# Kernel optimization log

Hardware: AMD Instinct MI355X
Metric: run time of the kernel (lower is better)

Reference implementation:

```python
import jax, jax.numpy as jnp
import numpy as np

B, T = 16384, 128
PI = np.pi
MAX_ITERS = 1000


def _quat_to_mat(q):
    # pytorch3d quaternion_to_matrix, q is (..., 4) wxyz
    w, x, y, z = q[..., 0], q[..., 1], q[..., 2], q[..., 3]
    two = 2.0 / jnp.sum(q * q, axis=-1)
    r00 = 1.0 - two * (y * y + z * z)
    r01 = two * (x * y - z * w)
    r02 = two * (x * z + y * w)
    r10 = two * (x * y + z * w)
    r11 = 1.0 - two * (x * x + z * z)
    r12 = two * (y * z - x * w)
    r20 = two * (x * z - y * w)
    r21 = two * (y * z + x * w)
    r22 = 1.0 - two * (x * x + y * y)
    return jnp.stack([
        jnp.stack([r00, r01, r02], -1),
        jnp.stack([r10, r11, r12], -1),
        jnp.stack([r20, r21, r22], -1)], -2)


def _mat_to_quat(m):
    # pytorch3d matrix_to_quaternion, m is (..., 3, 3) -> (..., 4) wxyz
    m00, m01, m02 = m[..., 0, 0], m[..., 0, 1], m[..., 0, 2]
    m10, m11, m12 = m[..., 1, 0], m[..., 1, 1], m[..., 1, 2]
    m20, m21, m22 = m[..., 2, 0], m[..., 2, 1], m[..., 2, 2]
    q_abs = jnp.sqrt(jnp.clip(jnp.stack([
        1.0 + m00 + m11 + m22,
        1.0 + m00 - m11 - m22,
        1.0 - m00 + m11 - m22,
        1.0 - m00 - m11 + m22], -1), 1e-8))
    cand = jnp.stack([
        jnp.stack([q_abs[..., 0] ** 2, m21 - m12, m02 - m20, m10 - m01], -1),
        jnp.stack([m21 - m12, q_abs[..., 1] ** 2, m01 + m10, m02 + m20], -1),
        jnp.stack([m02 - m20, m10 + m01, q_abs[..., 2] ** 2, m12 + m21], -1),
        jnp.stack([m10 - m01, m20 + m02, m21 + m12, q_abs[..., 3] ** 2], -1)], -2)
    cand = cand / (2.0 * jnp.maximum(q_abs[..., None], 0.1))
    best = jnp.argmax(q_abs, axis=-1)
    return jnp.take_along_axis(cand, best[..., None, None], axis=-2)[..., 0, :]


def _build_R(key, batch, dtype):
    k = jax.random.split(key, 4)
    ax = jax.random.uniform(k[0], (batch,), dtype) * 2 * PI - PI
    ay = jax.random.uniform(k[1], (batch,), dtype) * 2 * PI - PI
    az = jax.random.uniform(k[2], (batch,), dtype) * 2 * PI - PI
    mask = jax.random.uniform(k[3], (batch,), dtype) < (1.0 / 64.0)
    ax = jnp.where(mask, 0.0, ax)
    ay = jnp.where(mask, 0.0, ay)
    az = jnp.where(mask, 0.0, az)
    cx, sx = jnp.cos(ax), jnp.sin(ax)
    cy, sy = jnp.cos(ay), jnp.sin(ay)
    cz, sz = jnp.cos(az), jnp.sin(az)
    o, z0 = jnp.ones_like(ax), jnp.zeros_like(ax)
    Rx = jnp.stack([jnp.stack([o, z0, z0], -1), jnp.stack([z0, cx, -sx], -1), jnp.stack([z0, sx, cx], -1)], -2)
    Ry = jnp.stack([jnp.stack([cy, z0, sy], -1), jnp.stack([z0, o, z0], -1), jnp.stack([-sy, z0, cy], -1)], -2)
    Rz = jnp.stack([jnp.stack([cz, -sz, z0], -1), jnp.stack([sz, cz, z0], -1), jnp.stack([z0, z0, o], -1)], -2)
    return Rz @ Ry @ Rx  # [B, 3, 3]


def setup_inputs() -> dict:
    key = jax.random.key(0)
    kp, kq = jax.random.split(key)
    # positions scaled to (-0.5, 0.5): every point has norm < 1 so rotated
    # components stay in [-1, 1] and the acceptance test passes
    pos = (jax.random.uniform(kp, (B, T, 3), jnp.float32) * 2.0 - 1.0) * 0.5
    quat = jax.random.normal(kq, (B, T, 4), jnp.float32)
    quat = quat / jnp.linalg.norm(quat, axis=-1, keepdims=True)
    return {"pos": pos, "quat": quat}


def reference(pos, quat):
    batch = pos.shape[0]
    quat_wxyz = quat[..., jnp.array([3, 0, 1, 2])]
    eye = jnp.broadcast_to(jnp.eye(3, dtype=pos.dtype), (batch, 3, 3))

    def cond(s):
        i, key, acc, R = s
        return jnp.logical_and(~acc, i < MAX_ITERS)

    def body(s):
        i, key, acc, R = s
        key, sub = jax.random.split(key)
        Rn = _build_R(sub, batch, pos.dtype)
        rp = jnp.einsum('bij,btj->bti', Rn, pos)
        ok = jnp.logical_and(rp.min() >= -1.0, rp.max() <= 1.0)
        return (i + 1, key, ok, Rn)

    i, _, acc, R = jax.lax.while_loop(
        cond, body, (jnp.int32(0), jax.random.key(42), jnp.bool_(False), eye))
    # torch code falls back to identity if it exhausted all 1000 tries
    # (including acceptance on the very last iteration, matching `if i == 999`)
    use_id = i >= MAX_ITERS
    Rf = jnp.where(use_id, eye, R)
    rotated_pos = jnp.einsum('bij,btj->bti', Rf, pos)
    rot = _quat_to_mat(quat_wxyz)                       # [B,T,3,3]
    rotated_rot = jnp.einsum('bij,btjk->btik', Rf, rot)
    rotated_quat = _mat_to_quat(rotated_rot)[..., jnp.array([1, 2, 3, 0])]  # back to xyzw
    pos_out = jnp.where(use_id, pos, rotated_pos)
    quat_out = jnp.where(use_id, quat, rotated_quat)
    return pos_out, quat_out, Rf
```

## Files before the change

### kernel.cpp

```cpp
#include <hip/hip_runtime.h>
#include <stdint.h>

#define B_DIM 16384
#define T_DIM 128

struct U2 { uint32_t a, b; };

__host__ __device__ constexpr uint32_t rotl32c(uint32_t x, uint32_t n) {
    return (x << n) | (x >> (32u - n));
}

__host__ __device__ constexpr U2 tf(uint32_t k0, uint32_t k1,
                                    uint32_t x0, uint32_t x1) {
    uint32_t ks2 = k0 ^ k1 ^ 0x1BD11BDAu;
    x0 += k0; x1 += k1;
#define RND(r) { x0 += x1; x1 = rotl32c(x1, r); x1 ^= x0; }
    RND(13) RND(15) RND(26) RND(6)
    x0 += k1; x1 += ks2 + 1u;
    RND(17) RND(29) RND(16) RND(24)
    x0 += ks2; x1 += k0 + 2u;
    RND(13) RND(15) RND(26) RND(6)
    x0 += k0; x1 += k1 + 3u;
    RND(17) RND(29) RND(16) RND(24)
    x0 += k1; x1 += ks2 + 4u;
    RND(13) RND(15) RND(26) RND(6)
    x0 += ks2; x1 += k0 + 5u;
#undef RND
    return U2{x0, x1};
}

constexpr U2 SUB = tf(0u, 42u, 0u, 1u);
constexpr U2 K0 = tf(SUB.a, SUB.b, 0u, 0u);
constexpr U2 K1 = tf(SUB.a, SUB.b, 0u, 1u);
constexpr U2 K2 = tf(SUB.a, SUB.b, 0u, 2u);
constexpr U2 K3 = tf(SUB.a, SUB.b, 0u, 3u);

__device__ __forceinline__ float bits_to_uniform(uint32_t bits) {
    uint32_t u = (bits >> 9) | 0x3F800000u;
    return __uint_as_float(u) - 1.0f;
}

__device__ __forceinline__ uint32_t rbits(U2 k, uint32_t i) {
    U2 o = tf(k.a, k.b, 0u, i);
    return o.a ^ o.b;
}

__global__ void build_R_kernel(float* __restrict__ Rf) {
    int b = blockIdx.x * blockDim.x + threadIdx.x;
    if (b >= B_DIM) return;

    uint32_t bx = rbits(K0, (uint32_t)b);
    uint32_t by = rbits(K1, (uint32_t)b);
    uint32_t bz = rbits(K2, (uint32_t)b);
    uint32_t bm = rbits(K3, (uint32_t)b);

    const float PI_F = 3.14159265358979323846f;
    float ax = bits_to_uniform(bx) * 2.0f * PI_F - PI_F;
    float ay = bits_to_uniform(by) * 2.0f * PI_F - PI_F;
    float az = bits_to_uniform(bz) * 2.0f * PI_F - PI_F;
    bool mask = bits_to_uniform(bm) < 0.015625f;
    if (mask) { ax = 0.0f; ay = 0.0f; az = 0.0f; }

    float sx, cx, sy, cy, sz, cz;
    sincosf(ax, &sx, &cx);
    sincosf(ay, &sy, &cy);
    sincosf(az, &sz, &cz);

    float r00 = cz * cy;
    float r01 = cz * sy * sx - sz * cx;
    float r02 = cz * sy * cx + sz * sx;
    float r10 = sz * cy;
    float r11 = sz * sy * sx + cz * cx;
    float r12 = sz * sy * cx - cz * sx;
    float r20 = -sy;
    float r21 = cy * sx;
    float r22 = cy * cx;

    float* o = Rf + (size_t)b * 9;
    o[0] = r00; o[1] = r01; o[2] = r02;
    o[3] = r10; o[4] = r11; o[5] = r12;
    o[6] = r20; o[7] = r21; o[8] = r22;
}

__global__ __launch_bounds__(T_DIM) void rot_apply_kernel(
    const float* __restrict__ pos, const float* __restrict__ quat,
    const float* __restrict__ Rf, float* __restrict__ pos_out,
    float* __restrict__ quat_out) {
    __shared__ float Rs[9];
    int b = blockIdx.x;
    int t = threadIdx.x;
    if (t < 9) Rs[t] = Rf[(size_t)b * 9 + t];
    __syncthreads();
    float R00 = Rs[0], R01 = Rs[1], R02 = Rs[2];
    float R10 = Rs[3], R11 = Rs[4], R12 = Rs[5];
    float R20 = Rs[6], R21 = Rs[7], R22 = Rs[8];

    size_t idx = (size_t)b * T_DIM + t;

    const float* p = pos + idx * 3;
    float px = p[0], py = p[1], pz = p[2];
    float ox = R00 * px + R01 * py + R02 * pz;
    float oy = R10 * px + R11 * py + R12 * pz;
    float oz = R20 * px + R21 * py + R22 * pz;
    float* po = pos_out + idx * 3;
    po[0] = ox; po[1] = oy; po[2] = oz;

    float4 q = ((const float4*)quat)[idx];
    float qx = q.x, qy = q.y, qz = q.z, qw = q.w;
    float ss = qw * qw + qx * qx + qy * qy + qz * qz;
    float two = 2.0f / ss;
    float m00 = 1.0f - two * (qy * qy + qz * qz);
    float m01 = two * (qx * qy - qz * qw);
    float m02 = two * (qx * qz + qy * qw);
    float m10 = two * (qx * qy + qz * qw);
    float m11 = 1.0f - two * (qx * qx + qz * qz);
    float m12 = two * (qy * qz - qx * qw);
    float m20 = two * (qx * qz - qy * qw);
    float m21 = two * (qy * qz + qx * qw);
    float m22 = 1.0f - two * (qx * qx + qy * qy);

    float n00 = R00 * m00 + R01 * m10 + R02 * m20;
    float n01 = R00 * m01 + R01 * m11 + R02 * m21;
    float n02 = R00 * m02 + R01 * m12 + R02 * m22;
    float n10 = R10 * m00 + R11 * m10 + R12 * m20;
    float n11 = R10 * m01 + R11 * m11 + R12 * m21;
    float n12 = R10 * m02 + R11 * m12 + R12 * m22;
    float n20 = R20 * m00 + R21 * m10 + R22 * m20;
    float n21 = R20 * m01 + R21 * m11 + R22 * m21;
    float n22 = R20 * m02 + R21 * m12 + R22 * m22;

    float t0 = 1.0f + n00 + n11 + n22;
    float t1 = 1.0f + n00 - n11 - n22;
    float t2 = 1.0f - n00 + n11 - n22;
    float t3 = 1.0f - n00 - n11 + n22;
    float q0 = sqrtf(fmaxf(t0, 1e-8f));
    float q1 = sqrtf(fmaxf(t1, 1e-8f));
    float q2 = sqrtf(fmaxf(t2, 1e-8f));
    float q3 = sqrtf(fmaxf(t3, 1e-8f));

    int best = 0; float bv = q0;
    if (q1 > bv) { best = 1; bv = q1; }
    if (q2 > bv) { best = 2; bv = q2; }
    if (q3 > bv) { best = 3; bv = q3; }
    float denom = 2.0f * fmaxf(bv, 0.1f);

    float w, x, y, z;
    if (best == 0)      { w = q0 * q0;  x = n21 - n12; y = n02 - n20; z = n10 - n01; }
    else if (best == 1) { w = n21 - n12; x = q1 * q1;  y = n01 + n10; z = n02 + n20; }
    else if (best == 2) { w = n02 - n20; x = n10 + n01; y = q2 * q2;  z = n12 + n21; }
    else                { w = n10 - n01; x = n20 + n02; y = n21 + n12; z = q3 * q3;  }

    float4 qo;
    qo.x = x / denom; qo.y = y / denom; qo.z = z / denom; qo.w = w / denom;
    ((float4*)quat_out)[idx] = qo;
}

extern "C" void kernel_launch(void* const* d_in, const int* in_sizes, int n_in,
                              void* d_out, int out_size, void* d_ws, size_t ws_size,
                              hipStream_t stream) {
    const float* pos  = (const float*)d_in[0];
    const float* quat = (const float*)d_in[1];
    float* out = (float*)d_out;
    float* pos_out  = out;
    float* quat_out = out + (size_t)B_DIM * T_DIM * 3;
    float* Rf       = out + (size_t)B_DIM * T_DIM * 7;

    build_R_kernel<<<(B_DIM + 255) / 256, 256, 0, stream>>>(Rf);
    rot_apply_kernel<<<B_DIM, T_DIM, 0, stream>>>(pos, quat, Rf, pos_out, quat_out);
}
```

Measured before the change: 110.5 us.

## Stage pos through LDS for coalesced float4 I/O and process two batches per block

The apply kernel now loads each batch's position data into shared memory with float4 reads and writes the rotated positions back through shared memory as float4 stores. This replaces strided 3-float accesses per thread. Each block handles two batch rows with 256 threads. The build kernel uses 64-thread blocks to spread work over more CUs, and the four quaternion divides become one reciprocal plus multiplies. The cost is a second barrier and extra LDS traffic.

```diff
diff --git a/kernel.cpp b/kernel.cpp
--- a/kernel.cpp
+++ b/kernel.cpp
@@ -3,6 +3,8 @@
 
 #define B_DIM 16384
 #define T_DIM 128
+#define NB 2
+#define BLK (NB * T_DIM)
 
 struct U2 { uint32_t a, b; };
 
@@ -45,7 +47,7 @@
     return o.a ^ o.b;
 }
 
-__global__ void build_R_kernel(float* __restrict__ Rf) {
+__global__ __launch_bounds__(64) void build_R_kernel(float* __restrict__ Rf) {
     int b = blockIdx.x * blockDim.x + threadIdx.x;
     if (b >= B_DIM) return;
 
@@ -82,28 +84,36 @@
     o[6] = r20; o[7] = r21; o[8] = r22;
 }
 
-__global__ __launch_bounds__(T_DIM) void rot_apply_kernel(
+__global__ __launch_bounds__(BLK) void rot_apply_kernel(
     const float* __restrict__ pos, const float* __restrict__ quat,
     const float* __restrict__ Rf, float* __restrict__ pos_out,
     float* __restrict__ quat_out) {
-    __shared__ float Rs[9];
-    int b = blockIdx.x;
-    int t = threadIdx.x;
-    if (t < 9) Rs[t] = Rf[(size_t)b * 9 + t];
+    __shared__ float Ps[NB * T_DIM * 3];
+    __shared__ float Rs[NB * 9];
+
+    const int t  = threadIdx.x;
+    const int b0 = blockIdx.x * NB;
+
+    if (t < NB * 9) Rs[t] = Rf[(size_t)b0 * 9 + t];
+
+    const float4* pin = (const float4*)(pos + (size_t)b0 * T_DIM * 3);
+    if (t < NB * T_DIM * 3 / 4) ((float4*)Ps)[t] = pin[t];
     __syncthreads();
-    float R00 = Rs[0], R01 = Rs[1], R02 = Rs[2];
-    float R10 = Rs[3], R11 = Rs[4], R12 = Rs[5];
-    float R20 = Rs[6], R21 = Rs[7], R22 = Rs[8];
 
-    size_t idx = (size_t)b * T_DIM + t;
+    const int lb = t >> 7;
+    const int e  = t & (T_DIM - 1);
+    const size_t idx = (size_t)(b0 + lb) * T_DIM + e;
+    const int pofs = lb * (T_DIM * 3) + e * 3;
 
-    const float* p = pos + idx * 3;
-    float px = p[0], py = p[1], pz = p[2];
-    float ox = R00 * px + R01 * py + R02 * pz;
-    float oy = R10 * px + R11 * py + R12 * pz;
-    float oz = R20 * px + R21 * py + R22 * pz;
-    float* po = pos_out + idx * 3;
-    po[0] = ox; po[1] = oy; po[2] = oz;
+    const float* Rb = Rs + lb * 9;
+    const float R00 = Rb[0], R01 = Rb[1], R02 = Rb[2];
+    const float R10 = Rb[3], R11 = Rb[4], R12 = Rb[5];
+    const float R20 = Rb[6], R21 = Rb[7], R22 = Rb[8];
+
+    const float px = Ps[pofs + 0], py = Ps[pofs + 1], pz = Ps[pofs + 2];
+    const float ox = R00 * px + R01 * py + R02 * pz;
+    const float oy = R10 * px + R11 * py + R12 * pz;
+    const float oz = R20 * px + R21 * py + R22 * pz;
 
     float4 q = ((const float4*)quat)[idx];
     float qx = q.x, qy = q.y, qz = q.z, qw = q.w;
@@ -142,7 +152,6 @@
     if (q1 > bv) { best = 1; bv = q1; }
     if (q2 > bv) { best = 2; bv = q2; }
     if (q3 > bv) { best = 3; bv = q3; }
-    float denom = 2.0f * fmaxf(bv, 0.1f);
 
     float w, x, y, z;
     if (best == 0)      { w = q0 * q0;  x = n21 - n12; y = n02 - n20; z = n10 - n01; }
@@ -150,9 +159,15 @@
     else if (best == 2) { w = n02 - n20; x = n10 + n01; y = q2 * q2;  z = n12 + n21; }
     else                { w = n10 - n01; x = n20 + n02; y = n21 + n12; z = q3 * q3;  }
 
+    const float inv = 1.0f / (2.0f * fmaxf(bv, 0.1f));
     float4 qo;
-    qo.x = x / denom; qo.y = y / denom; qo.z = z / denom; qo.w = w / denom;
+    qo.x = x * inv; qo.y = y * inv; qo.z = z * inv; qo.w = w * inv;
     ((float4*)quat_out)[idx] = qo;
+
+    Ps[pofs + 0] = ox; Ps[pofs + 1] = oy; Ps[pofs + 2] = oz;
+    __syncthreads();
+    float4* pout = (float4*)(pos_out + (size_t)b0 * T_DIM * 3);
+    if (t < NB * T_DIM * 3 / 4) pout[t] = ((float4*)Ps)[t];
 }
 
 extern "C" void kernel_launch(void* const* d_in, const int* in_sizes, int n_in,
@@ -165,6 +180,6 @@
     float* quat_out = out + (size_t)B_DIM * T_DIM * 3;
     float* Rf       = out + (size_t)B_DIM * T_DIM * 7;
 
-    build_R_kernel<<<(B_DIM + 255) / 256, 256, 0, stream>>>(Rf);
-    rot_apply_kernel<<<B_DIM, T_DIM, 0, stream>>>(pos, quat, Rf, pos_out, quat_out);
+    build_R_kernel<<<B_DIM / 64, 64, 0, stream>>>(Rf);
+    rot_apply_kernel<<<B_DIM / NB, BLK, 0, stream>>>(pos, quat, Rf, pos_out, quat_out);
 }
```

After: 108.1 us. -2.1%, faster.
